# Kernel optimization log

Hardware: AMD Instinct MI355X
Metric: run time of the kernel (lower is better)

Reference implementation:

```python
import jax, jax.numpy as jnp
import numpy as np

N_NODES = 100000
N_EDGES = 1600000
N_GRAPHS = 256
SEQ = 365
F_DYN = 16
F_STAT = 32
H_GNN = 64
H_RNN = 128
EPS = 1e-5  # BatchNorm eps (eval mode, running stats)


def _bn(x, g, b, m, v):
    return (x - m) * jax.lax.rsqrt(v + EPS) * g + b


def _gcn(x, src, dst, W, b, n):
    # PyG GCNConv: linear -> sym-normalized aggregation with self-loops -> bias
    h = x @ W  # [n, out]
    deg = jnp.ones((n,), h.dtype).at[dst].add(1.0)  # in-degree + self-loop
    dinv = jax.lax.rsqrt(deg)
    norm = dinv[src] * dinv[dst]  # [E]
    agg = jnp.zeros_like(h).at[dst].add(h[src] * norm[:, None])
    agg = agg + h * (dinv * dinv)[:, None]  # self-loop contribution
    return agg + b


def _lstm_layer(x, Wih, Whh, bih, bhh):
    # torch nn.LSTM gate order: i, f, g, o; Wih [4H, in], Whh [4H, H]
    B = x.shape[0]
    H = Whh.shape[1]
    def step(carry, xt):
        h, c = carry
        z = xt @ Wih.T + h @ Whh.T + bih + bhh
        i, f, g, o = jnp.split(z, 4, axis=-1)
        c = jax.nn.sigmoid(f) * c + jax.nn.sigmoid(i) * jnp.tanh(g)
        h = jax.nn.sigmoid(o) * jnp.tanh(c)
        return (h, c), h
    init = (jnp.zeros((B, H), x.dtype), jnp.zeros((B, H), x.dtype))
    _, hs = jax.lax.scan(step, init, jnp.swapaxes(x, 0, 1))
    return jnp.swapaxes(hs, 0, 1)


def setup_inputs() -> dict:
    key = jax.random.key(0)
    ks = jax.random.split(key, 40)
    def rn(i, shape, scale=1.0):
        return jax.random.normal(ks[i], shape, jnp.float32) * scale
    inp = {}
    inp['dynamic_features'] = rn(0, (N_GRAPHS, SEQ, F_DYN))
    inp['x_static'] = rn(1, (N_NODES, F_STAT))
    inp['edge_index'] = jax.random.randint(ks[2], (2, N_EDGES), 0, N_NODES, jnp.int32)
    inp['batch_idx'] = jnp.sort(jax.random.randint(ks[3], (N_NODES,), 0, N_GRAPHS, jnp.int32))
    # GCN weights stored [in, out] (equivalent to torch [out, in] transposed)
    inp['W_g1'] = rn(4, (F_STAT, H_GNN), F_STAT ** -0.5)
    inp['b_g1'] = jnp.zeros((H_GNN,), jnp.float32)
    inp['W_g2'] = rn(5, (H_GNN, H_GNN), H_GNN ** -0.5)
    inp['b_g2'] = jnp.zeros((H_GNN,), jnp.float32)
    for i, name in [(6, 'bn1'), (7, 'bn2')]:
        inp[name + '_gamma'] = jnp.ones((H_GNN,), jnp.float32)
        inp[name + '_beta'] = jnp.zeros((H_GNN,), jnp.float32)
        inp[name + '_mean'] = rn(i, (H_GNN,), 0.1)
        inp[name + '_var'] = jax.random.uniform(ks[i + 10], (H_GNN,), jnp.float32) + 0.5
    G = 4 * H_RNN
    inp['lstm0_Wih'] = rn(8, (G, F_DYN), F_DYN ** -0.5)
    inp['lstm0_Whh'] = rn(9, (G, H_RNN), H_RNN ** -0.5)
    inp['lstm0_bih'] = jnp.zeros((G,), jnp.float32)
    inp['lstm0_bhh'] = jnp.zeros((G,), jnp.float32)
    inp['lstm1_Wih'] = rn(20, (G, H_RNN), H_RNN ** -0.5)
    inp['lstm1_Whh'] = rn(21, (G, H_RNN), H_RNN ** -0.5)
    inp['lstm1_bih'] = jnp.zeros((G,), jnp.float32)
    inp['lstm1_bhh'] = jnp.zeros((G,), jnp.float32)
    F_FUSE = H_GNN + H_RNN
    inp['W_f1'] = rn(22, (F_FUSE, 128), F_FUSE ** -0.5)
    inp['b_f1'] = jnp.zeros((128,), jnp.float32)
    inp['fbn_gamma'] = jnp.ones((128,), jnp.float32)
    inp['fbn_beta'] = jnp.zeros((128,), jnp.float32)
    inp['fbn_mean'] = rn(23, (128,), 0.1)
    inp['fbn_var'] = jax.random.uniform(ks[24], (128,), jnp.float32) + 0.5
    inp['W_f2'] = rn(25, (128, 64), 128 ** -0.5)
    inp['b_f2'] = jnp.zeros((64,), jnp.float32)
    inp['W_out'] = rn(26, (64, 10), 64 ** -0.5)
    inp['b_out'] = jnp.zeros((10,), jnp.float32)
    return inp


def reference(dynamic_features, x_static, edge_index, batch_idx,
              W_g1, b_g1, W_g2, b_g2,
              bn1_gamma, bn1_beta, bn1_mean, bn1_var,
              bn2_gamma, bn2_beta, bn2_mean, bn2_var,
              lstm0_Wih, lstm0_Whh, lstm0_bih, lstm0_bhh,
              lstm1_Wih, lstm1_Whh, lstm1_bih, lstm1_bhh,
              W_f1, b_f1, fbn_gamma, fbn_beta, fbn_mean, fbn_var,
              W_f2, b_f2, W_out, b_out):
    src, dst = edge_index[0], edge_index[1]
    n = x_static.shape[0]
    # GNN branch (dropout is identity in eval)
    h = jax.nn.relu(_bn(_gcn(x_static, src, dst, W_g1, b_g1, n), bn1_gamma, bn1_beta, bn1_mean, bn1_var))
    h = jax.nn.relu(_bn(_gcn(h, src, dst, W_g2, b_g2, n), bn2_gamma, bn2_beta, bn2_mean, bn2_var))
    # global mean pool over graphs
    sums = jax.ops.segment_sum(h, batch_idx, num_segments=N_GRAPHS)
    cnt = jax.ops.segment_sum(jnp.ones((n,), h.dtype), batch_idx, num_segments=N_GRAPHS)
    gnn_emb = sums / jnp.maximum(cnt, 1.0)[:, None]
    # RNN branch: 2-layer LSTM, take last timestep
    r = _lstm_layer(dynamic_features, lstm0_Wih, lstm0_Whh, lstm0_bih, lstm0_bhh)
    r = _lstm_layer(r, lstm1_Wih, lstm1_Whh, lstm1_bih, lstm1_bhh)
    rnn_emb = r[:, -1, :]
    # Fusion head
    fused = jnp.concatenate([gnn_emb, rnn_emb], axis=1)
    x = jax.nn.relu(_bn(fused @ W_f1 + b_f1, fbn_gamma, fbn_beta, fbn_mean, fbn_var))
    x = jax.nn.relu(x @ W_f2 + b_f2)
    return x @ W_out + b_out
```

## Files before the change

kernel.cpp:

```cpp
#include <hip/hip_runtime.h>

#define N_NODES 100000
#define N_EDGES 1600000
#define N_GRAPHS 256
#define SEQ 365
#define F_DYN 16
#define H_GNN 64
#define GATES 512
#define EPSV 1e-5f
#define TC 48
#define NCHUNK 8
#define NBLK_SCAN 391

__device__ __forceinline__ float rl(float v, int l) {
    return __int_as_float(__builtin_amdgcn_readlane(__float_as_int(v), l));
}
__device__ __forceinline__ float sigmoidf_(float x) { return 1.f / (1.f + __expf(-x)); }
__device__ __forceinline__ float tanhf_(float x) { return 1.f - 2.f / (__expf(2.f * x) + 1.f); }


__global__ void hist_kernel(const int* __restrict__ ei, int* __restrict__ deg) {
    int e = blockIdx.x * 256 + threadIdx.x;
    if (e < N_EDGES) atomicAdd(&deg[ei[N_EDGES + e]], 1);
}

__global__ __launch_bounds__(256) void scan1_kernel(const int* __restrict__ deg, int* __restrict__ bsum) {
    __shared__ int sm[256];
    int n = blockIdx.x * 256 + threadIdx.x;
    sm[threadIdx.x] = (n < N_NODES) ? deg[n] : 0;
    __syncthreads();
    for (int off = 128; off > 0; off >>= 1) {
        if (threadIdx.x < off) sm[threadIdx.x] += sm[threadIdx.x + off];
        __syncthreads();
    }
    if (threadIdx.x == 0) bsum[blockIdx.x] = sm[0];
}

__global__ __launch_bounds__(512) void scan2_kernel(int* __restrict__ bsum) {
    __shared__ int sc[512];
    int tid = threadIdx.x;
    int v = (tid < NBLK_SCAN) ? bsum[tid] : 0;
    sc[tid] = v;
    __syncthreads();
    for (int off = 1; off < 512; off <<= 1) {
        int t = (tid >= off) ? sc[tid - off] : 0;
        __syncthreads();
        sc[tid] += t;
        __syncthreads();
    }
    if (tid < NBLK_SCAN) bsum[tid] = sc[tid] - v;
}

__global__ __launch_bounds__(256) void scan3_kernel(const int* __restrict__ deg, const int* __restrict__ bsum,
                                                    int* __restrict__ offs, int* __restrict__ cursor,
                                                    float* __restrict__ dinv) {
    __shared__ int sc[256];
    int tid = threadIdx.x, n = blockIdx.x * 256 + tid;
    int v = (n < N_NODES) ? deg[n] : 0;
    sc[tid] = v;
    __syncthreads();
    for (int off = 1; off < 256; off <<= 1) {
        int t = (tid >= off) ? sc[tid - off] : 0;
        __syncthreads();
        sc[tid] += t;
        __syncthreads();
    }
    int ex = sc[tid] - v + bsum[blockIdx.x];
    if (n < N_NODES) {
        offs[n] = ex;
        cursor[n] = ex;
        dinv[n] = rsqrtf(1.f + (float)v);
        if (n == N_NODES - 1) offs[N_NODES] = ex + v;
    }
}

__global__ void fill_kernel(const int* __restrict__ ei, const float* __restrict__ dinv,
                            int* __restrict__ cursor, int2* __restrict__ epk) {
    int e = blockIdx.x * 256 + threadIdx.x;
    if (e >= N_EDGES) return;
    int s = ei[e], d = ei[N_EDGES + e];
    int pos = atomicAdd(&cursor[d], 1);
    epk[pos] = make_int2(s, __float_as_int(dinv[s] * dinv[d]));
}


template <int K>
__global__ __launch_bounds__(256) void mm_kernel(const float* __restrict__ X,
                                                 const float* __restrict__ W,
                                                 float* __restrict__ P) {
    __shared__ float Xs[64 * K];
    __shared__ float Ws[K * 64];
    int tid = threadIdx.x, bm = blockIdx.x;
#pragma unroll
    for (int i = 0; i < (K * 64 / 4) / 256; i++)
        ((float4*)Ws)[i * 256 + tid] = ((const float4*)W)[i * 256 + tid];
#pragma unroll
    for (int i = 0; i < (64 * K / 4) / 256; i++) {
        int f4 = i * 256 + tid;
        int r = (f4 * 4) / K, c = (f4 * 4) % K;
        int row = bm * 64 + r;
        float4 v = make_float4(0.f, 0.f, 0.f, 0.f);
        if (row < N_NODES) v = *(const float4*)(X + (size_t)row * K + c);
        ((float4*)Xs)[f4] = v;
    }
    __syncthreads();
    int f = tid & 63, nz = tid >> 6;
    float acc[16];
#pragma unroll
    for (int i = 0; i < 16; i++) acc[i] = 0.f;
    for (int k = 0; k < K; k++) {
        float wv = Ws[k * 64 + f];
#pragma unroll
        for (int ni = 0; ni < 16; ni++) acc[ni] += Xs[(nz * 16 + ni) * K + k] * wv;
    }
#pragma unroll
    for (int ni = 0; ni < 16; ni++) {
        int row = bm * 64 + nz * 16 + ni;
        if (row < N_NODES) P[(size_t)row * 64 + f] = acc[ni];
    }
}

__global__ __launch_bounds__(256) void gather_kernel(const float* __restrict__ P,
                                                     const int2* __restrict__ epk,
                                                     const int* __restrict__ offs,
                                                     const float* __restrict__ dinv,
                                                     const float* __restrict__ bias,
                                                     const float* __restrict__ gm, const float* __restrict__ bt,
                                                     const float* __restrict__ mn, const float* __restrict__ vr,
                                                     float* __restrict__ H) {
    int node = blockIdx.x * 4 + (threadIdx.x >> 6);
    int f = threadIdx.x & 63;
    float di = dinv[node];
    int beg = offs[node], end = offs[node + 1];
    float acc0 = P[(size_t)node * 64 + f] * di * di;
    float acc1 = 0.f;
    int i = beg;
    for (; i + 1 < end; i += 2) {
        int2 e0 = epk[i], e1 = epk[i + 1];
        acc0 += P[(size_t)e0.x * 64 + f] * __int_as_float(e0.y);
        acc1 += P[(size_t)e1.x * 64 + f] * __int_as_float(e1.y);
    }
    if (i < end) {
        int2 e0 = epk[i];
        acc0 += P[(size_t)e0.x * 64 + f] * __int_as_float(e0.y);
    }
    float vv = acc0 + acc1 + bias[f];
    float s = gm[f] * rsqrtf(vr[f] + EPSV);
    vv = (vv - mn[f]) * s + bt[f];
    H[(size_t)node * 64 + f] = fmaxf(vv, 0.f);
}

__global__ __launch_bounds__(256) void pool_kernel(const float* __restrict__ H,
                                                   const int* __restrict__ batch,
                                                   float* __restrict__ emb) {
    int g = blockIdx.x, tid = threadIdx.x;
    int lo = 0, hi = N_NODES;
    while (lo < hi) { int mid = (lo + hi) >> 1; if (batch[mid] < g) lo = mid + 1; else hi = mid; }
    int start = lo;
    hi = N_NODES;
    while (lo < hi) { int mid = (lo + hi) >> 1; if (batch[mid] < g + 1) lo = mid + 1; else hi = mid; }
    int end = lo;
    int f = tid & 63, p = tid >> 6;
    float acc = 0.f;
    for (int n = start + p; n < end; n += 4) acc += H[(size_t)n * 64 + f];
    __shared__ float sm[4][64];
    sm[p][f] = acc;
    __syncthreads();
    if (p == 0) {
        float tot = sm[0][f] + sm[1][f] + sm[2][f] + sm[3][f];
        emb[g * 64 + f] = tot / fmaxf((float)(end - start), 1.f);
    }
}


__global__ __launch_bounds__(512, 2) void lstm0_kernel(const float* __restrict__ dyn,
                                                       const float* __restrict__ Wih,
                                                       const float* __restrict__ Whh,
                                                       const float* __restrict__ bih,
                                                       const float* __restrict__ bhh,
                                                       float* __restrict__ H0) {
    int b = blockIdx.x, g = threadIdx.x, lane = g & 63;
    float w[128];
    const float4* W4 = (const float4*)(Whh + (size_t)g * 128);
#pragma unroll
    for (int i = 0; i < 32; i++) {
        float4 v = W4[i];
        w[4 * i] = v.x; w[4 * i + 1] = v.y; w[4 * i + 2] = v.z; w[4 * i + 3] = v.w;
    }
    float wx[16];
    const float4* Wx4 = (const float4*)(Wih + (size_t)g * 16);
#pragma unroll
    for (int i = 0; i < 4; i++) {
        float4 v = Wx4[i];
        wx[4 * i] = v.x; wx[4 * i + 1] = v.y; wx[4 * i + 2] = v.z; wx[4 * i + 3] = v.w;
    }
    float bias = bih[g] + bhh[g];
    __shared__ float h_s[128];
    __shared__ float z_s[512];
    float c = 0.f;
    if (g < 128) h_s[g] = 0.f;
    __syncthreads();
    const float* xb = dyn + (size_t)b * SEQ * F_DYN;
    float* Hb = H0 + (size_t)b * SEQ * 128;
    float xtv = xb[lane & 15];
    for (int t = 0; t < SEQ; t++) {
        float xtn = (t + 1 < SEQ) ? xb[(t + 1) * 16 + (lane & 15)] : 0.f;
        float hva = h_s[lane], hvb = h_s[64 + lane];
        float a0 = bias, a1 = 0.f, a2 = 0.f, a3 = 0.f;
#pragma unroll
        for (int k = 0; k < 16; k += 4) {
            a0 += wx[k] * rl(xtv, k);
            a1 += wx[k + 1] * rl(xtv, k + 1);
            a2 += wx[k + 2] * rl(xtv, k + 2);
            a3 += wx[k + 3] * rl(xtv, k + 3);
        }
#pragma unroll
        for (int k = 0; k < 64; k += 4) {
            a0 += w[k] * rl(hva, k);
            a1 += w[k + 1] * rl(hva, k + 1);
            a2 += w[k + 2] * rl(hva, k + 2);
            a3 += w[k + 3] * rl(hva, k + 3);
        }
#pragma unroll
        for (int k = 0; k < 64; k += 4) {
            a0 += w[64 + k] * rl(hvb, k);
            a1 += w[65 + k] * rl(hvb, k + 1);
            a2 += w[66 + k] * rl(hvb, k + 2);
            a3 += w[67 + k] * rl(hvb, k + 3);
        }
        z_s[g] = (a0 + a1) + (a2 + a3);
        __syncthreads();
        if (g < 128) {
            float zi = z_s[g], zf = z_s[g + 128], zg = z_s[g + 256], zo = z_s[g + 384];
            float ii = sigmoidf_(zi), ff = sigmoidf_(zf), gg = tanhf_(zg), oo = sigmoidf_(zo);
            c = ff * c + ii * gg;
            float hn = oo * tanhf_(c);
            h_s[g] = hn;
            Hb[t * 128 + g] = hn;
        }
        __syncthreads();
        xtv = xtn;
    }
}

__global__ __launch_bounds__(256, 2) void gemm_a1_kernel(const float* __restrict__ H0,
                                                         const float* __restrict__ B,
                                                         const float* __restrict__ bih,
                                                         const float* __restrict__ bhh,
                                                         float* __restrict__ A1c, int t0) {
    __shared__ float As[64][132];
    __shared__ float Bs[64][132];
    int tid = threadIdx.x;
    int bm = blockIdx.x, bn = blockIdx.y;
    int tx = tid & 15, ty = tid >> 4;
    float acc[8][8];
#pragma unroll
    for (int i = 0; i < 8; i++)
#pragma unroll
        for (int j = 0; j < 8; j++) acc[i][j] = 0.f;
    for (int kc = 0; kc < 128; kc += 64) {
#pragma unroll
        for (int i = 0; i < 8; i++) {
            int f4 = i * 256 + tid;
            int r = f4 >> 4;
            int cc = (f4 & 15) * 4;
            int row = bm * 128 + r;
            int bb = row / TC, tl = row - bb * TC;
            int t = t0 + tl;
            float4 v = make_float4(0.f, 0.f, 0.f, 0.f);
            if (t < SEQ) v = *(const float4*)(H0 + ((size_t)bb * SEQ + t) * 128 + kc + cc);
            As[cc + 0][r] = v.x; As[cc + 1][r] = v.y; As[cc + 2][r] = v.z; As[cc + 3][r] = v.w;
            float4 u = *(const float4*)(B + (size_t)(bn * 128 + r) * 128 + kc + cc);
            Bs[cc + 0][r] = u.x; Bs[cc + 1][r] = u.y; Bs[cc + 2][r] = u.z; Bs[cc + 3][r] = u.w;
        }
        __syncthreads();
#pragma unroll
        for (int k = 0; k < 64; k++) {
            float av[8], bv[8];
            *(float4*)&av[0] = *(const float4*)&As[k][ty * 8];
            *(float4*)&av[4] = *(const float4*)&As[k][ty * 8 + 4];
            *(float4*)&bv[0] = *(const float4*)&Bs[k][tx * 8];
            *(float4*)&bv[4] = *(const float4*)&Bs[k][tx * 8 + 4];
#pragma unroll
            for (int i = 0; i < 8; i++)
#pragma unroll
                for (int j = 0; j < 8; j++) acc[i][j] += av[i] * bv[j];
        }
        __syncthreads();
    }
    float bb8[8];
#pragma unroll
    for (int j = 0; j < 8; j++) {
        int col = bn * 128 + tx * 8 + j;
        bb8[j] = bih[col] + bhh[col];
    }
#pragma unroll
    for (int i = 0; i < 8; i++) {
        int row = bm * 128 + ty * 8 + i;
        float4 o0 = make_float4(acc[i][0] + bb8[0], acc[i][1] + bb8[1], acc[i][2] + bb8[2], acc[i][3] + bb8[3]);
        float4 o1 = make_float4(acc[i][4] + bb8[4], acc[i][5] + bb8[5], acc[i][6] + bb8[6], acc[i][7] + bb8[7]);
        *(float4*)(A1c + (size_t)row * GATES + bn * 128 + tx * 8) = o0;
        *(float4*)(A1c + (size_t)row * GATES + bn * 128 + tx * 8 + 4) = o1;
    }
}

__global__ __launch_bounds__(512, 2) void lstm1_kernel(const float* __restrict__ A1c,
                                                       const float* __restrict__ Whh,
                                                       float* __restrict__ state,
                                                       float* __restrict__ rnn, int t0, int tc) {
    int b = blockIdx.x, g = threadIdx.x, lane = g & 63;
    float w[128];
    const float4* W4 = (const float4*)(Whh + (size_t)g * 128);
#pragma unroll
    for (int i = 0; i < 32; i++) {
        float4 v = W4[i];
        w[4 * i] = v.x; w[4 * i + 1] = v.y; w[4 * i + 2] = v.z; w[4 * i + 3] = v.w;
    }
    __shared__ float h_s[128];
    __shared__ float z_s[512];
    float c = 0.f;
    if (g < 128) {
        if (t0 == 0) {
            h_s[g] = 0.f;
        } else {
            h_s[g] = state[b * 128 + g];
            c = state[N_GRAPHS * 128 + b * 128 + g];
        }
    }
    __syncthreads();
    const float* Ab = A1c + (size_t)b * TC * GATES;
    float a_cur = Ab[g];
    float hn = 0.f;
    for (int tl = 0; tl < tc; tl++) {
        float a_next = (tl + 1 < tc) ? Ab[(tl + 1) * GATES + g] : 0.f;
        float hva = h_s[lane], hvb = h_s[64 + lane];
        float a0 = a_cur, a1 = 0.f, a2 = 0.f, a3 = 0.f;
#pragma unroll
        for (int k = 0; k < 64; k += 4) {
            a0 += w[k] * rl(hva, k);
            a1 += w[k + 1] * rl(hva, k + 1);
            a2 += w[k + 2] * rl(hva, k + 2);
            a3 += w[k + 3] * rl(hva, k + 3);
        }
#pragma unroll
        for (int k = 0; k < 64; k += 4) {
            a0 += w[64 + k] * rl(hvb, k);
            a1 += w[65 + k] * rl(hvb, k + 1);
            a2 += w[66 + k] * rl(hvb, k + 2);
            a3 += w[67 + k] * rl(hvb, k + 3);
        }
        z_s[g] = (a0 + a1) + (a2 + a3);
        __syncthreads();
        if (g < 128) {
            float zi = z_s[g], zf = z_s[g + 128], zg = z_s[g + 256], zo = z_s[g + 384];
            float ii = sigmoidf_(zi), ff = sigmoidf_(zf), gg = tanhf_(zg), oo = sigmoidf_(zo);
            c = ff * c + ii * gg;
            hn = oo * tanhf_(c);
            h_s[g] = hn;
        }
        __syncthreads();
        a_cur = a_next;
    }
    if (g < 128) {
        state[b * 128 + g] = hn;
        state[N_GRAPHS * 128 + b * 128 + g] = c;
        if (t0 + tc == SEQ) rnn[b * 128 + g] = hn;
    }
}


__global__ __launch_bounds__(128) void head_kernel(const float* __restrict__ gnn, const float* __restrict__ rnn,
                                                   const float* __restrict__ Wf1, const float* __restrict__ bf1,
                                                   const float* __restrict__ fg, const float* __restrict__ fb,
                                                   const float* __restrict__ fm, const float* __restrict__ fv,
                                                   const float* __restrict__ Wf2, const float* __restrict__ bf2,
                                                   const float* __restrict__ Wo, const float* __restrict__ bo,
                                                   float* __restrict__ out) {
    int b = blockIdx.x, tid = threadIdx.x;
    __shared__ float fused[192];
    __shared__ float x1[128];
    __shared__ float x2[64];
    if (tid < 64) fused[tid] = gnn[b * 64 + tid];
    fused[64 + tid] = rnn[b * 128 + tid];
    __syncthreads();
    float acc = bf1[tid];
    for (int k = 0; k < 192; k++) acc += fused[k] * Wf1[k * 128 + tid];
    float s = fg[tid] * rsqrtf(fv[tid] + EPSV);
    acc = (acc - fm[tid]) * s + fb[tid];
    x1[tid] = fmaxf(acc, 0.f);
    __syncthreads();
    if (tid < 64) {
        float a2 = bf2[tid];
        for (int k = 0; k < 128; k++) a2 += x1[k] * Wf2[k * 64 + tid];
        x2[tid] = fmaxf(a2, 0.f);
    }
    __syncthreads();
    if (tid < 10) {
        float a3 = bo[tid];
        for (int k = 0; k < 64; k++) a3 += x2[k] * Wo[k * 10 + tid];
        out[b * 10 + tid] = a3;
    }
}

extern "C" void kernel_launch(void* const* d_in, const int* in_sizes, int n_in,
                              void* d_out, int out_size, void* d_ws, size_t ws_size,
                              hipStream_t stream) {
    const float* dyn = (const float*)d_in[0];
    const float* xs = (const float*)d_in[1];
    const int* ei = (const int*)d_in[2];
    const int* batch = (const int*)d_in[3];
    const float* Wg1 = (const float*)d_in[4];
    const float* bg1 = (const float*)d_in[5];
    const float* Wg2 = (const float*)d_in[6];
    const float* bg2 = (const float*)d_in[7];
    const float* bn1g = (const float*)d_in[8], *bn1b = (const float*)d_in[9];
    const float* bn1m = (const float*)d_in[10], *bn1v = (const float*)d_in[11];
    const float* bn2g = (const float*)d_in[12], *bn2b = (const float*)d_in[13];
    const float* bn2m = (const float*)d_in[14], *bn2v = (const float*)d_in[15];
    const float* l0Wih = (const float*)d_in[16], *l0Whh = (const float*)d_in[17];
    const float* l0bih = (const float*)d_in[18], *l0bhh = (const float*)d_in[19];
    const float* l1Wih = (const float*)d_in[20], *l1Whh = (const float*)d_in[21];
    const float* l1bih = (const float*)d_in[22], *l1bhh = (const float*)d_in[23];
    const float* Wf1 = (const float*)d_in[24], *bf1 = (const float*)d_in[25];
    const float* fbg = (const float*)d_in[26], *fbb = (const float*)d_in[27];
    const float* fbm = (const float*)d_in[28], *fbv = (const float*)d_in[29];
    const float* Wf2 = (const float*)d_in[30], *bf2 = (const float*)d_in[31];
    const float* Wo = (const float*)d_in[32], *bo = (const float*)d_in[33];
    float* out = (float*)d_out;

    float* ws = (float*)d_ws;
    float* P = ws;
    float* H = P + 6400000;
    float* dinv = H + 6400000;
    float* gnn = dinv + 100000;
    float* rnn = gnn + 16384;
    float* st = rnn + 32768;
    float* H0 = st + 65536;
    float* A1c = H0 + 11962880;
    int* deg = (int*)(A1c + 6291456);
    int* offs = deg + 100096;
    int* cursor = offs + 100001;
    int* bsum = cursor + 100001;
    int2* epk = (int2*)(bsum + 512);

    hipMemsetAsync(deg, 0, N_NODES * sizeof(int), stream);
    hist_kernel<<<(N_EDGES + 255) / 256, 256, 0, stream>>>(ei, deg);
    scan1_kernel<<<NBLK_SCAN, 256, 0, stream>>>(deg, bsum);
    scan2_kernel<<<1, 512, 0, stream>>>(bsum);
    scan3_kernel<<<NBLK_SCAN, 256, 0, stream>>>(deg, bsum, offs, cursor, dinv);
    fill_kernel<<<(N_EDGES + 255) / 256, 256, 0, stream>>>(ei, dinv, cursor, epk);

    mm_kernel<32><<<(N_NODES + 63) / 64, 256, 0, stream>>>(xs, Wg1, P);
    gather_kernel<<<N_NODES / 4, 256, 0, stream>>>(P, epk, offs, dinv, bg1, bn1g, bn1b, bn1m, bn1v, H);
    mm_kernel<64><<<(N_NODES + 63) / 64, 256, 0, stream>>>(H, Wg2, P);
    gather_kernel<<<N_NODES / 4, 256, 0, stream>>>(P, epk, offs, dinv, bg2, bn2g, bn2b, bn2m, bn2v, H);

    pool_kernel<<<N_GRAPHS, 256, 0, stream>>>(H, batch, gnn);

    lstm0_kernel<<<N_GRAPHS, 512, 0, stream>>>(dyn, l0Wih, l0Whh, l0bih, l0bhh, H0);
    for (int ch = 0; ch < NCHUNK; ch++) {
        int t0 = ch * TC;
        int tc = (SEQ - t0 < TC) ? (SEQ - t0) : TC;
        gemm_a1_kernel<<<dim3(96, 4), 256, 0, stream>>>(H0, l1Wih, l1bih, l1bhh, A1c, t0);
        lstm1_kernel<<<N_GRAPHS, 512, 0, stream>>>(A1c, l1Whh, st, rnn, t0, tc);
    }

    head_kernel<<<N_GRAPHS, 128, 0, stream>>>(gnn, rnn, Wf1, bf1, fbg, fbb, fbm, fbv, Wf2, bf2, Wo, bo, out);
}
```

Measured before the change: 1.835 ms.

## Overlap GCN branch with LSTM on side streams and pack LSTM FMAs

Moves the GCN pipeline onto a separate non-blocking stream so it runs concurrently with the LSTM recurrence. Moves the layer-1 input GEMM onto another stream, with double-buffered A1 chunks, so the next chunk's GEMM can overlap the current lstm1 recurrence. The recurrent matvecs in both LSTM kernels now use 2-wide vector FMAs, which may map to packed FP32 FMA instructions and halve the FMA issue count. The cost is extra events, cross-stream synchronisation, and a workspace-size dependence for double buffering.

```diff
diff --git a/kernel.cpp b/kernel.cpp
--- a/kernel.cpp
+++ b/kernel.cpp
@@ -12,11 +12,33 @@
 #define NCHUNK 8
 #define NBLK_SCAN 391
 
+typedef float v2f __attribute__((ext_vector_type(2)));
+#define FMA2(a, b, c) __builtin_elementwise_fma((a), (b), (c))
+
 __device__ __forceinline__ float rl(float v, int l) {
     return __int_as_float(__builtin_amdgcn_readlane(__float_as_int(v), l));
 }
 __device__ __forceinline__ float sigmoidf_(float x) { return 1.f / (1.f + __expf(-x)); }
 __device__ __forceinline__ float tanhf_(float x) { return 1.f - 2.f / (__expf(2.f * x) + 1.f); }
+
+static hipStream_t s_gcn = nullptr, s_gemm = nullptr;
+static hipEvent_t evFork = nullptr, evH0 = nullptr, evGCN = nullptr;
+static hipEvent_t evG[NCHUNK], evL[NCHUNK];
+static bool g_ok = false;
+static struct SideInit {
+    SideInit() {
+        g_ok = true;
+        if (hipStreamCreateWithFlags(&s_gcn, hipStreamNonBlocking) != hipSuccess) g_ok = false;
+        if (hipStreamCreateWithFlags(&s_gemm, hipStreamNonBlocking) != hipSuccess) g_ok = false;
+        if (hipEventCreateWithFlags(&evFork, hipEventDisableTiming) != hipSuccess) g_ok = false;
+        if (hipEventCreateWithFlags(&evH0, hipEventDisableTiming) != hipSuccess) g_ok = false;
+        if (hipEventCreateWithFlags(&evGCN, hipEventDisableTiming) != hipSuccess) g_ok = false;
+        for (int i = 0; i < NCHUNK; i++) {
+            if (hipEventCreateWithFlags(&evG[i], hipEventDisableTiming) != hipSuccess) g_ok = false;
+            if (hipEventCreateWithFlags(&evL[i], hipEventDisableTiming) != hipSuccess) g_ok = false;
+        }
+    }
+} s_side_init;
 
 
 __global__ void hist_kernel(const int* __restrict__ ei, int* __restrict__ deg) {
@@ -180,19 +202,21 @@
                                                        const float* __restrict__ bhh,
                                                        float* __restrict__ H0) {
     int b = blockIdx.x, g = threadIdx.x, lane = g & 63;
-    float w[128];
+    v2f w2[64];
     const float4* W4 = (const float4*)(Whh + (size_t)g * 128);
 #pragma unroll
     for (int i = 0; i < 32; i++) {
         float4 v = W4[i];
-        w[4 * i] = v.x; w[4 * i + 1] = v.y; w[4 * i + 2] = v.z; w[4 * i + 3] = v.w;
-    }
-    float wx[16];
+        w2[2 * i] = (v2f){v.x, v.y};
+        w2[2 * i + 1] = (v2f){v.z, v.w};
+    }
+    v2f wx2[8];
     const float4* Wx4 = (const float4*)(Wih + (size_t)g * 16);
 #pragma unroll
     for (int i = 0; i < 4; i++) {
         float4 v = Wx4[i];
-        wx[4 * i] = v.x; wx[4 * i + 1] = v.y; wx[4 * i + 2] = v.z; wx[4 * i + 3] = v.w;
+        wx2[2 * i] = (v2f){v.x, v.y};
+        wx2[2 * i + 1] = (v2f){v.z, v.w};
     }
     float bias = bih[g] + bhh[g];
     __shared__ float h_s[128];
@@ -206,29 +230,23 @@
     for (int t = 0; t < SEQ; t++) {
         float xtn = (t + 1 < SEQ) ? xb[(t + 1) * 16 + (lane & 15)] : 0.f;
         float hva = h_s[lane], hvb = h_s[64 + lane];
-        float a0 = bias, a1 = 0.f, a2 = 0.f, a3 = 0.f;
+        v2f acc0 = (v2f){bias, 0.f}, acc1 = (v2f){0.f, 0.f};
 #pragma unroll
         for (int k = 0; k < 16; k += 4) {
-            a0 += wx[k] * rl(xtv, k);
-            a1 += wx[k + 1] * rl(xtv, k + 1);
-            a2 += wx[k + 2] * rl(xtv, k + 2);
-            a3 += wx[k + 3] * rl(xtv, k + 3);
+            acc0 = FMA2(wx2[k >> 1], ((v2f){rl(xtv, k), rl(xtv, k + 1)}), acc0);
+            acc1 = FMA2(wx2[(k >> 1) + 1], ((v2f){rl(xtv, k + 2), rl(xtv, k + 3)}), acc1);
         }
 #pragma unroll
         for (int k = 0; k < 64; k += 4) {
-            a0 += w[k] * rl(hva, k);
-            a1 += w[k + 1] * rl(hva, k + 1);
-            a2 += w[k + 2] * rl(hva, k + 2);
-            a3 += w[k + 3] * rl(hva, k + 3);
+            acc0 = FMA2(w2[k >> 1], ((v2f){rl(hva, k), rl(hva, k + 1)}), acc0);
+            acc1 = FMA2(w2[(k >> 1) + 1], ((v2f){rl(hva, k + 2), rl(hva, k + 3)}), acc1);
         }
 #pragma unroll
         for (int k = 0; k < 64; k += 4) {
-            a0 += w[64 + k] * rl(hvb, k);
-            a1 += w[65 + k] * rl(hvb, k + 1);
-            a2 += w[66 + k] * rl(hvb, k + 2);
-            a3 += w[67 + k] * rl(hvb, k + 3);
-        }
-        z_s[g] = (a0 + a1) + (a2 + a3);
+            acc0 = FMA2(w2[32 + (k >> 1)], ((v2f){rl(hvb, k), rl(hvb, k + 1)}), acc0);
+            acc1 = FMA2(w2[32 + (k >> 1) + 1], ((v2f){rl(hvb, k + 2), rl(hvb, k + 3)}), acc1);
+        }
+        z_s[g] = (acc0.x + acc0.y) + (acc1.x + acc1.y);
         __syncthreads();
         if (g < 128) {
             float zi = z_s[g], zf = z_s[g + 128], zg = z_s[g + 256], zo = z_s[g + 384];
@@ -309,12 +327,13 @@
                                                        float* __restrict__ state,
                                                        float* __restrict__ rnn, int t0, int tc) {
     int b = blockIdx.x, g = threadIdx.x, lane = g & 63;
-    float w[128];
+    v2f w2[64];
     const float4* W4 = (const float4*)(Whh + (size_t)g * 128);
 #pragma unroll
     for (int i = 0; i < 32; i++) {
         float4 v = W4[i];
-        w[4 * i] = v.x; w[4 * i + 1] = v.y; w[4 * i + 2] = v.z; w[4 * i + 3] = v.w;
+        w2[2 * i] = (v2f){v.x, v.y};
+        w2[2 * i + 1] = (v2f){v.z, v.w};
     }
     __shared__ float h_s[128];
     __shared__ float z_s[512];
@@ -334,22 +353,18 @@
     for (int tl = 0; tl < tc; tl++) {
         float a_next = (tl + 1 < tc) ? Ab[(tl + 1) * GATES + g] : 0.f;
         float hva = h_s[lane], hvb = h_s[64 + lane];
-        float a0 = a_cur, a1 = 0.f, a2 = 0.f, a3 = 0.f;
+        v2f acc0 = (v2f){a_cur, 0.f}, acc1 = (v2f){0.f, 0.f};
 #pragma unroll
         for (int k = 0; k < 64; k += 4) {
-            a0 += w[k] * rl(hva, k);
-            a1 += w[k + 1] * rl(hva, k + 1);
-            a2 += w[k + 2] * rl(hva, k + 2);
-            a3 += w[k + 3] * rl(hva, k + 3);
+            acc0 = FMA2(w2[k >> 1], ((v2f){rl(hva, k), rl(hva, k + 1)}), acc0);
+            acc1 = FMA2(w2[(k >> 1) + 1], ((v2f){rl(hva, k + 2), rl(hva, k + 3)}), acc1);
         }
 #pragma unroll
         for (int k = 0; k < 64; k += 4) {
-            a0 += w[64 + k] * rl(hvb, k);
-            a1 += w[65 + k] * rl(hvb, k + 1);
-            a2 += w[66 + k] * rl(hvb, k + 2);
-            a3 += w[67 + k] * rl(hvb, k + 3);
-        }
-        z_s[g] = (a0 + a1) + (a2 + a3);
+            acc0 = FMA2(w2[32 + (k >> 1)], ((v2f){rl(hvb, k), rl(hvb, k + 1)}), acc0);
+            acc1 = FMA2(w2[32 + (k >> 1) + 1], ((v2f){rl(hvb, k + 2), rl(hvb, k + 3)}), acc1);
+        }
+        z_s[g] = (acc0.x + acc0.y) + (acc1.x + acc1.y);
         __syncthreads();
         if (g < 128) {
             float zi = z_s[g], zf = z_s[g + 128], zg = z_s[g + 256], zo = z_s[g + 384];
@@ -442,28 +457,59 @@
     int* cursor = offs + 100001;
     int* bsum = cursor + 100001;
     int2* epk = (int2*)(bsum + 512);
-
-    hipMemsetAsync(deg, 0, N_NODES * sizeof(int), stream);
-    hist_kernel<<<(N_EDGES + 255) / 256, 256, 0, stream>>>(ei, deg);
-    scan1_kernel<<<NBLK_SCAN, 256, 0, stream>>>(deg, bsum);
-    scan2_kernel<<<1, 512, 0, stream>>>(bsum);
-    scan3_kernel<<<NBLK_SCAN, 256, 0, stream>>>(deg, bsum, offs, cursor, dinv);
-    fill_kernel<<<(N_EDGES + 255) / 256, 256, 0, stream>>>(ei, dinv, cursor, epk);
-
-    mm_kernel<32><<<(N_NODES + 63) / 64, 256, 0, stream>>>(xs, Wg1, P);
-    gather_kernel<<<N_NODES / 4, 256, 0, stream>>>(P, epk, offs, dinv, bg1, bn1g, bn1b, bn1m, bn1v, H);
-    mm_kernel<64><<<(N_NODES + 63) / 64, 256, 0, stream>>>(H, Wg2, P);
-    gather_kernel<<<N_NODES / 4, 256, 0, stream>>>(P, epk, offs, dinv, bg2, bn2g, bn2b, bn2m, bn2v, H);
-
-    pool_kernel<<<N_GRAPHS, 256, 0, stream>>>(H, batch, gnn);
+    float* A1c2 = (float*)(epk + N_EDGES);
+
+    const size_t NEED_DB = ((size_t)(A1c2 - ws) + 6291456) * 4;
+    bool MS = g_ok && s_gcn && s_gemm;
+    bool DB = MS && ws_size >= NEED_DB;
+    float* A1buf[2] = {A1c, DB ? A1c2 : A1c};
+
+    hipStream_t sg = MS ? s_gcn : stream;
+    hipStream_t sm = MS ? s_gemm : stream;
+
+    if (MS) {
+        hipEventRecord(evFork, stream);
+        hipStreamWaitEvent(sg, evFork, 0);
+    }
+
+    hipMemsetAsync(deg, 0, N_NODES * sizeof(int), sg);
+    hist_kernel<<<(N_EDGES + 255) / 256, 256, 0, sg>>>(ei, deg);
+    scan1_kernel<<<NBLK_SCAN, 256, 0, sg>>>(deg, bsum);
+    scan2_kernel<<<1, 512, 0, sg>>>(bsum);
+    scan3_kernel<<<NBLK_SCAN, 256, 0, sg>>>(deg, bsum, offs, cursor, dinv);
+    fill_kernel<<<(N_EDGES + 255) / 256, 256, 0, sg>>>(ei, dinv, cursor, epk);
+    mm_kernel<32><<<(N_NODES + 63) / 64, 256, 0, sg>>>(xs, Wg1, P);
+    gather_kernel<<<N_NODES / 4, 256, 0, sg>>>(P, epk, offs, dinv, bg1, bn1g, bn1b, bn1m, bn1v, H);
+    mm_kernel<64><<<(N_NODES + 63) / 64, 256, 0, sg>>>(H, Wg2, P);
+    gather_kernel<<<N_NODES / 4, 256, 0, sg>>>(P, epk, offs, dinv, bg2, bn2g, bn2b, bn2m, bn2v, H);
+    pool_kernel<<<N_GRAPHS, 256, 0, sg>>>(H, batch, gnn);
+    if (MS) hipEventRecord(evGCN, sg);
 
     lstm0_kernel<<<N_GRAPHS, 512, 0, stream>>>(dyn, l0Wih, l0Whh, l0bih, l0bhh, H0);
+    if (MS) {
+        hipEventRecord(evH0, stream);
+        hipStreamWaitEvent(sm, evH0, 0);
+    }
     for (int ch = 0; ch < NCHUNK; ch++) {
         int t0 = ch * TC;
         int tc = (SEQ - t0 < TC) ? (SEQ - t0) : TC;
-        gemm_a1_kernel<<<dim3(96, 4), 256, 0, stream>>>(H0, l1Wih, l1bih, l1bhh, A1c, t0);
-        lstm1_kernel<<<N_GRAPHS, 512, 0, stream>>>(A1c, l1Whh, st, rnn, t0, tc);
-    }
-
+        float* Ab = A1buf[ch & 1];
+        if (MS) {
+            if (DB) {
+                if (ch >= 2) hipStreamWaitEvent(sm, evL[ch - 2], 0);
+            } else {
+                if (ch >= 1) hipStreamWaitEvent(sm, evL[ch - 1], 0);
+            }
+        }
+        gemm_a1_kernel<<<dim3(96, 4), 256, 0, sm>>>(H0, l1Wih, l1bih, l1bhh, Ab, t0);
+        if (MS) {
+            hipEventRecord(evG[ch], sm);
+            hipStreamWaitEvent(stream, evG[ch], 0);
+        }
+        lstm1_kernel<<<N_GRAPHS, 512, 0, stream>>>(Ab, l1Whh, st, rnn, t0, tc);
+        if (MS) hipEventRecord(evL[ch], stream);
+    }
+
+    if (MS) hipStreamWaitEvent(stream, evGCN, 0);
     head_kernel<<<N_GRAPHS, 128, 0, stream>>>(gnn, rnn, Wf1, bf1, fbg, fbb, fbm, fbv, Wf2, bf2, Wo, bo, out);
 }
```

After: 1.996 ms. 8.7% more time.
